# Kernel optimization log

Measured on AMD Instinct MI355X. Metric: run time of the kernel, lower is better.

## Reference

```python
import jax, jax.numpy as jnp
import numpy as np

B, T, S, E, H, V, OOV = 16, 32, 400, 128, 512, 32000, 50


def setup_inputs() -> dict:
    key = jax.random.key(0)
    ks = jax.random.split(key, 24)
    sc = 0.05
    inp = {
        'input_embeddings': jax.random.normal(ks[0], (B, T, E), jnp.float32),
        'h0': jax.random.normal(ks[1], (B, H), jnp.float32) * sc,
        'c0': jax.random.normal(ks[2], (B, H), jnp.float32) * sc,
        'encoder_outputs': jax.random.normal(ks[3], (B, S, H), jnp.float32),
        'encoder_masks': jnp.ones((B, S), jnp.float32),
        'extra_zeros': jnp.zeros((B, OOV), jnp.float32),
        'extended_source_idx': jax.random.randint(ks[4], (B, S), 0, V + OOV),
        # LSTM cell params (torch gate order i,f,g,o)
        'W_ih': jax.random.normal(ks[5], (4 * H, E), jnp.float32) * sc,
        'W_hh': jax.random.normal(ks[6], (4 * H, H), jnp.float32) * sc,
        'b_ih': jax.random.normal(ks[7], (4 * H,), jnp.float32) * sc,
        'b_hh': jax.random.normal(ks[8], (4 * H,), jnp.float32) * sc,
        # vocab projection
        'W_vocab': jax.random.normal(ks[9], (V, H), jnp.float32) * sc,
        'b_vocab': jax.random.normal(ks[10], (V,), jnp.float32) * sc,
        # attention: coverage_linear (H,1), energy_linear (H, 2H), v (H)
        'W_cov': jax.random.normal(ks[11], (H, 1), jnp.float32) * sc,
        'W_energy': jax.random.normal(ks[12], (H, 2 * H), jnp.float32) * sc,
        'b_energy': jax.random.normal(ks[13], (H,), jnp.float32) * sc,
        'v_attn': jax.random.uniform(ks[14], (H,), jnp.float32),
        # x_context: (E, E+H)
        'W_xctx': jax.random.normal(ks[15], (E, E + H), jnp.float32) * sc,
        'b_xctx': jax.random.normal(ks[16], (E,), jnp.float32) * sc,
        # attention_dense: (H, 2H)
        'W_ad': jax.random.normal(ks[17], (H, 2 * H), jnp.float32) * sc,
        'b_ad': jax.random.normal(ks[18], (H,), jnp.float32) * sc,
        # p_gen: (1, H + H + E)
        'W_pgen': jax.random.normal(ks[19], (1, 2 * H + E), jnp.float32) * sc,
        'b_pgen': jax.random.normal(ks[20], (1,), jnp.float32) * sc,
    }
    return inp


def _forward(input_embeddings, h0, c0, encoder_outputs, encoder_masks, extra_zeros,
             W_ih, W_hh, b_ih, b_hh, W_vocab, b_vocab, W_cov, W_energy, b_energy,
             v_attn, W_xctx, b_xctx, W_ad, b_ad, W_pgen, b_pgen, extended_source_idx):
    Bc, Sc_, Hc = encoder_outputs.shape
    oov = extra_zeros.shape[1]
    # split energy linear into decoder-part and encoder-part (cat order: [dec, enc])
    W_d, W_e = W_energy[:, :Hc], W_energy[:, Hc:]
    # encoder projection computed ONCE (same math as per-step recompute)
    enc_proj = jnp.einsum('bsh,kh->bsk', encoder_outputs, W_e) + b_energy  # [B,S,H]
    w_cov = W_cov[:, 0]  # [H]
    rows = jnp.arange(Bc)[:, None]

    def step(carry, emb_t):
        h, c, ctx, cov = carry  # [B,H],[B,H],[B,H],[B,S]
        x = jnp.concatenate([emb_t, ctx], -1) @ W_xctx.T + b_xctx  # [B,E]
        gates = x @ W_ih.T + b_ih + h @ W_hh.T + b_hh
        i_g, f_g, g_g, o_g = jnp.split(gates, 4, axis=-1)
        c = jax.nn.sigmoid(f_g) * c + jax.nn.sigmoid(i_g) * jnp.tanh(g_g)
        h = jax.nn.sigmoid(o_g) * jnp.tanh(c)
        # additive attention with coverage
        dec_proj = h @ W_d.T  # [B,H]
        cov_feat = cov[:, :, None] * w_cov[None, None, :]  # [B,S,H]
        energy = jnp.tanh(dec_proj[:, None, :] + enc_proj + cov_feat)
        score = jnp.einsum('bsh,h->bs', energy, v_attn)
        probs = jax.nn.softmax(score, axis=-1) * encoder_masks
        probs = probs / (probs.sum(-1, keepdims=True) + 1e-12)
        ctx = jnp.einsum('bs,bsh->bh', probs, encoder_outputs)
        cov = cov + probs
        # vocab distribution
        hh = jnp.concatenate([h, ctx], -1) @ W_ad.T + b_ad
        vocab_dist = jax.nn.softmax(hh @ W_vocab.T + b_vocab, axis=-1)  # [B,V]
        # pointer-generator mix
        p_gen = jax.nn.sigmoid(jnp.concatenate([ctx, h, x], -1) @ W_pgen.T + b_pgen)  # [B,1]
        attn_ = (1.0 - p_gen) * probs  # [B,S]
        ext = jnp.concatenate([vocab_dist * p_gen, extra_zeros], axis=1)  # [B,V+oov]
        final = ext.at[rows, extended_source_idx].add(attn_)
        return (h, c, ctx, cov), (final, probs, cov)

    init = (h0, c0, jnp.zeros_like(h0), jnp.zeros((Bc, Sc_), h0.dtype))
    (_, _, _, _), (finals, attns, covs) = jax.lax.scan(
        step, init, jnp.swapaxes(input_embeddings, 0, 1))
    return jnp.swapaxes(finals, 0, 1)  # [B,T,V+oov]


def reference(input_embeddings, h0, c0, encoder_outputs, encoder_masks, extra_zeros,
              extended_source_idx, W_ih, W_hh, b_ih, b_hh, W_vocab, b_vocab,
              W_cov, W_energy, b_energy, v_attn, W_xctx, b_xctx, W_ad, b_ad,
              W_pgen, b_pgen):
    return _forward(input_embeddings, h0, c0, encoder_outputs, encoder_masks,
                    extra_zeros, W_ih, W_hh, b_ih, b_hh, W_vocab, b_vocab,
                    W_cov, W_energy, b_energy, v_attn, W_xctx, b_xctx,
                    W_ad, b_ad, W_pgen, b_pgen, extended_source_idx)
```

## Files before the change

### kernel.cpp

```cpp
#include <hip/hip_runtime.h>
#include <hip/hip_bf16.h>
#include <cstddef>

namespace {

constexpr int B = 16, T = 32, S = 400, E = 128, H = 512, V = 32000, OOV = 50, VEXT = V + OOV;

typedef __attribute__((ext_vector_type(8))) short short8v;
typedef __attribute__((ext_vector_type(4))) float f32x4;

__device__ __forceinline__ float fsig(float x){ return 1.0f/(1.0f+__expf(-x)); }
__device__ __forceinline__ float ftanh(float x){
  float ax = fabsf(x);
  float t = __expf(-2.0f*ax);
  float r = (1.0f - t)/(1.0f + t);
  return copysignf(r, x);
}
__device__ __forceinline__ unsigned short f2bf(float f){
  unsigned int u = __float_as_uint(f);
  unsigned int r = (u + 0x7FFFu + ((u >> 16) & 1u)) >> 16;
  return (unsigned short)r;
}

__global__ __launch_bounds__(256) void k_init(const float* __restrict__ h0, const float* __restrict__ c0,
    float* __restrict__ h, float* __restrict__ c, float* __restrict__ cov,
    float* __restrict__ praw, float* __restrict__ vsum, float* __restrict__ hh_all){
  const int stride = gridDim.x*256;
  for (int i = blockIdx.x*256 + threadIdx.x; i < T*B*H; i += stride){
    hh_all[i] = 0.0f;
    if (i < B*H){ h[i]=h0[i]; c[i]=c0[i]; }
    if (i < B*S) cov[i]=0.0f;
    if (i < T*B){ praw[i]=0.0f; vsum[i]=0.0f; }
  }
}

__global__ __launch_bounds__(128) void k_x0(const float* __restrict__ emb,
    const float* __restrict__ W_xctx, const float* __restrict__ b_xctx,
    float* __restrict__ x0){
  const int b = blockIdx.x, tid = threadIdx.x;
  __shared__ float se[E];
  se[tid] = emb[(size_t)(b*T)*E + tid];
  __syncthreads();
  const float* w = W_xctx + (size_t)tid*(E+H);
  float acc = b_xctx[tid];
  #pragma unroll 8
  for (int k=0;k<E;k+=4){
    float4 wv = *reinterpret_cast<const float4*>(w+k);
    acc += se[k]*wv.x + se[k+1]*wv.y + se[k+2]*wv.z + se[k+3]*wv.w;
  }
  x0[b*E + tid] = acc;
}

__global__ __launch_bounds__(256) void k_trw2(const float* __restrict__ W_energy,
    float* __restrict__ Wt, float* __restrict__ WdT){
  __shared__ float tile[32][33];
  const int z = blockIdx.z;
  float* out = z ? WdT : Wt;
  const int off = z ? 0 : H;
  const int j0 = blockIdx.x*32, k0 = blockIdx.y*32;
  const int tx = threadIdx.x & 31, ty = threadIdx.x >> 5;
  #pragma unroll
  for (int r=0;r<4;++r)
    tile[ty+8*r][tx] = W_energy[(size_t)(k0+ty+8*r)*(2*H) + off + j0 + tx];
  __syncthreads();
  #pragma unroll
  for (int r=0;r<4;++r)
    out[(size_t)(j0+ty+8*r)*H + k0 + tx] = tile[tx][ty+8*r];
}

__global__ __launch_bounds__(512) void k_encproj(const float* __restrict__ enc,
                          const float* __restrict__ Wt,
                          const float* __restrict__ b_energy,
                          float* __restrict__ enc_proj){
  const int r0 = blockIdx.x*16, k = threadIdx.x;
  const float* eb = enc + (size_t)r0*H;
  float acc[16];
  #pragma unroll
  for (int r=0;r<16;++r) acc[r]=0.0f;
  for (int j=0;j<H;j+=4){
    const float w0 = Wt[(size_t) j   *H + k];
    const float w1 = Wt[(size_t)(j+1)*H + k];
    const float w2 = Wt[(size_t)(j+2)*H + k];
    const float w3 = Wt[(size_t)(j+3)*H + k];
    #pragma unroll
    for (int r=0;r<16;++r){
      acc[r] += eb[(size_t)r*H + j]*w0 + eb[(size_t)r*H + j+1]*w1
              + eb[(size_t)r*H + j+2]*w2 + eb[(size_t)r*H + j+3]*w3;
    }
  }
  const float be = b_energy[k];
  #pragma unroll
  for (int r=0;r<16;++r) enc_proj[(size_t)(r0+r)*H + k] = acc[r] + be;
}

__global__ __launch_bounds__(256) void k_gates2(
    const float* __restrict__ x, const float* __restrict__ hold,
    const float* __restrict__ W_ih, const float* __restrict__ W_hh,
    float* __restrict__ gpart){
  const int blk = blockIdx.x, tid = threadIdx.x;
  const int gbh = blk >> 2, kh = blk & 3;
  const int gb = gbh >> 1, bh = gbh & 1, b0 = bh*8;
  __shared__ float xh[8][640];
  __shared__ float sg[4][64][9];
  for (int b=0;b<8;++b)
    for (int k=tid;k<640;k+=256)
      xh[b][k] = (k<E) ? x[(b0+b)*E + k] : hold[(b0+b)*H + (k-E)];
  __syncthreads();
  const int w = tid >> 6, l = tid & 63, g = l >> 4, jj = l & 15;
  const int row = g*H + gb*16 + jj;
  float acc[8];
  #pragma unroll
  for (int b=0;b<8;++b) acc[b]=0.0f;
  const int ks = kh*160 + w*40, ke = ks + 40;
  const int k1 = (ke < 128) ? ke : 128;
  if (ks < 128){
    const float* wr = W_ih + (size_t)row*E;
    for (int k=ks; k<k1; k+=4){
      const float4 wv = *reinterpret_cast<const float4*>(wr + k);
      #pragma unroll
      for (int b=0;b<8;++b){
        const float4 xv = *reinterpret_cast<const float4*>(&xh[b][k]);
        acc[b] += xv.x*wv.x + xv.y*wv.y + xv.z*wv.z + xv.w*wv.w;
      }
    }
  }
  const int k2 = (ks > 128) ? ks : 128;
  if (k2 < ke){
    const float* wr = W_hh + (size_t)row*H - 128;
    for (int k=k2; k<ke; k+=4){
      const float4 wv = *reinterpret_cast<const float4*>(wr + k);
      #pragma unroll
      for (int b=0;b<8;++b){
        const float4 xv = *reinterpret_cast<const float4*>(&xh[b][k]);
        acc[b] += xv.x*wv.x + xv.y*wv.y + xv.z*wv.z + xv.w*wv.w;
      }
    }
  }
  #pragma unroll
  for (int b=0;b<8;++b) sg[w][l][b] = acc[b];
  __syncthreads();
  for (int i=tid; i<512; i+=256){
    const int l2 = i & 63, b = i >> 6;
    const int g2 = l2 >> 4, j2 = l2 & 15;
    const int row2 = g2*H + gb*16 + j2;
    gpart[((size_t)kh*B + (b0+b))*(4*H) + row2] =
        sg[0][l2][b]+sg[1][l2][b]+sg[2][l2][b]+sg[3][l2][b];
  }
}

__global__ __launch_bounds__(256) void k_dec2(const float* __restrict__ gpart,
    const float* __restrict__ cold, const float* __restrict__ b_ih,
    const float* __restrict__ b_hh, const float* __restrict__ WdT,
    float* __restrict__ cnew, float* __restrict__ hnew, float* __restrict__ dec){
  const int blk = blockIdx.x, tid = threadIdx.x;
  const int jc = blk >> 3, bp = blk & 7, b0 = bp*2;
  __shared__ float sh[2][H];
  __shared__ float r[4][64][2];
  for (int i=tid; i<2*H; i+=256){
    const int bl = i >> 9, j = i & 511;
    const int b = b0 + bl;
    float gs[4];
    #pragma unroll
    for (int g=0; g<4; ++g){
      const int row = g*H + j;
      float v = b_ih[row] + b_hh[row];
      #pragma unroll
      for (int kh=0; kh<4; ++kh) v += gpart[((size_t)kh*B + b)*(4*H) + row];
      gs[g] = v;
    }
    const float ig = fsig(gs[0]);
    const float fg = fsig(gs[1]);
    const float gg = ftanh(gs[2]);
    const float og = fsig(gs[3]);
    const float cn = fg*cold[b*H + j] + ig*gg;
    const float hn = og*ftanh(cn);
    cnew[b*H + j] = cn;
    hnew[b*H + j] = hn;
    sh[bl][j] = hn;
  }
  __syncthreads();
  const int w = tid >> 6, lane = tid & 63;
  const int j = jc*64 + lane;
  float a0=0.0f, a1=0.0f;
  for (int k=w*128; k<w*128+128; ++k){
    const float wv = WdT[(size_t)k*H + j];
    a0 += sh[0][k]*wv;
    a1 += sh[1][k]*wv;
  }
  r[w][lane][0]=a0; r[w][lane][1]=a1;
  __syncthreads();
  if (tid < 128){
    const int jl = tid & 63, bb = tid >> 6;
    dec[(b0+bb)*H + jc*64 + jl] = r[0][jl][bb]+r[1][jl][bb]+r[2][jl][bb]+r[3][jl][bb];
  }
}

__global__ __launch_bounds__(256) void k_score(const float* __restrict__ dec_proj,
    const float* __restrict__ enc_proj, const float* __restrict__ W_cov,
    const float* __restrict__ v_attn, const float* __restrict__ cov,
    float* __restrict__ score, float* __restrict__ xnext){
  const int b = blockIdx.y;
  if (blockIdx.x==0 && threadIdx.x < E) xnext[b*E + threadIdx.x] = 0.0f;
  const int wave = threadIdx.x >> 6, lane = threadIdx.x & 63;
  const int s = blockIdx.x*4 + wave;
  const float cv = cov[b*S + s];
  const float* ep = enc_proj + (size_t)(b*S + s)*H;
  const float* dp = dec_proj + b*H;
  float acc = 0.0f;
  const int k0 = lane*8;
  #pragma unroll
  for (int u=0;u<8;++u){
    const int k = k0+u;
    acc += ftanh(dp[k] + ep[k] + cv*W_cov[k]) * v_attn[k];
  }
  #pragma unroll
  for (int off=32; off>0; off>>=1) acc += __shfl_down(acc, off);
  if (lane==0) score[b*S + s] = acc;
}

__global__ __launch_bounds__(256) void k_ctxpost(const float* __restrict__ score,
    const float* __restrict__ masks, const float* __restrict__ enc,
    const float* __restrict__ h, const float* __restrict__ xcur,
    const float* __restrict__ emb, int tnext,
    const float* __restrict__ W_ad, const float* __restrict__ b_ad,
    const float* __restrict__ W_pgen, const float* __restrict__ b_pgen,
    const float* __restrict__ W_xctx, const float* __restrict__ b_xctx,
    float* __restrict__ cov, float* __restrict__ probs_t,
    float* __restrict__ hh_t, float* __restrict__ praw_t,
    float* __restrict__ xnext){
  const int b = blockIdx.x, hc = blockIdx.y, tid = threadIdx.x;
  __shared__ float red[256], sp[512], sctx[64], shh[H], se[E];
  for (int i=tid;i<H;i+=256) shh[i] = h[b*H + i];
  if (tid < E) se[tid] = emb[(size_t)(b*T + tnext)*E + tid];
  const float sc0 = (tid < S)      ? score[b*S + tid]       : -1e30f;
  const float sc1 = (tid+256 < S)  ? score[b*S + tid + 256] : -1e30f;
  red[tid] = fmaxf(sc0, sc1);
  __syncthreads();
  for (int off=128; off>0; off>>=1){ if (tid<off) red[tid]=fmaxf(red[tid],red[tid+off]); __syncthreads(); }
  const float mx = red[0];
  __syncthreads();
  const float e0 = (tid < S)     ? __expf(sc0 - mx) : 0.0f;
  const float e1 = (tid+256 < S) ? __expf(sc1 - mx) : 0.0f;
  red[tid] = e0 + e1;
  __syncthreads();
  for (int off=128; off>0; off>>=1){ if (tid<off) red[tid]+=red[tid+off]; __syncthreads(); }
  const float den = red[0];
  __syncthreads();
  const float p0 = (tid < S)     ? (e0/den)*masks[b*S+tid]     : 0.0f;
  const float p1 = (tid+256 < S) ? (e1/den)*masks[b*S+tid+256] : 0.0f;
  red[tid] = p0 + p1;
  __syncthreads();
  for (int off=128; off>0; off>>=1){ if (tid<off) red[tid]+=red[tid+off]; __syncthreads(); }
  const float inv = 1.0f/(red[0] + 1e-12f);
  __syncthreads();
  const float pr0 = p0*inv, pr1 = p1*inv;
  sp[tid] = pr0; sp[tid+256] = pr1;
  if (hc==0){
    if (tid < S){ probs_t[b*S+tid] = pr0; cov[b*S+tid] += pr0; }
    if (tid+256 < S){ probs_t[b*S+tid+256] = pr1; cov[b*S+tid+256] += pr1; }
  }
  __syncthreads();
  {
    const int c = tid & 63, sg_ = tid >> 6;
    const float* eb = enc + (size_t)b*S*H + hc*64 + c;
    float a = 0.0f;
    for (int s=sg_; s<S; s+=4) a += sp[s]*eb[(size_t)s*H];
    red[tid] = a;
    __syncthreads();
    if (tid < 64) sctx[tid] = red[tid]+red[tid+64]+red[tid+128]+red[tid+192];
  }
  __syncthreads();
  for (int j=tid; j<H; j+=256){
    const float* wr = W_ad + (size_t)j*(2*H);
    float acc = 0.0f;
    #pragma unroll
    for (int k=0;k<64;k+=4){
      const float4 wc = *reinterpret_cast<const float4*>(wr + H + hc*64 + k);
      acc += sctx[k]*wc.x + sctx[k+1]*wc.y + sctx[k+2]*wc.z + sctx[k+3]*wc.w;
      const float4 wh = *reinterpret_cast<const float4*>(wr + hc*64 + k);
      const float* hb = shh + hc*64 + k;
      acc += hb[0]*wh.x + hb[1]*wh.y + hb[2]*wh.z + hb[3]*wh.w;
    }
    if (hc==0) acc += b_ad[j];
    atomicAdd(&hh_t[b*H + j], acc);
  }
  if (tid < E){
    const float* wr = W_xctx + (size_t)tid*(E+H);
    float acc = 0.0f;
    #pragma unroll
    for (int k=0;k<64;k+=4){
      const float4 wc = *reinterpret_cast<const float4*>(wr + E + hc*64 + k);
      acc += sctx[k]*wc.x + sctx[k+1]*wc.y + sctx[k+2]*wc.z + sctx[k+3]*wc.w;
    }
    #pragma unroll
    for (int k=0;k<16;k+=4){
      const float4 we = *reinterpret_cast<const float4*>(wr + hc*16 + k);
      const float* eb2 = se + hc*16 + k;
      acc += eb2[0]*we.x + eb2[1]*we.y + eb2[2]*we.z + eb2[3]*we.w;
    }
    if (hc==0) acc += b_xctx[tid];
    atomicAdd(&xnext[b*E + tid], acc);
  }
  {
    float part = 0.0f;
    if (tid < 64){
      part = sctx[tid]*W_pgen[hc*64 + tid] + shh[hc*64 + tid]*W_pgen[H + hc*64 + tid];
      if (tid < 16) part += xcur[b*E + hc*16 + tid]*W_pgen[2*H + hc*16 + tid];
    }
    __syncthreads();
    red[tid] = part;
    __syncthreads();
    for (int off=128; off>0; off>>=1){ if (tid<off) red[tid]+=red[tid+off]; __syncthreads(); }
    if (tid==0) atomicAdd(&praw_t[b], red[0] + (hc==0 ? b_pgen[0] : 0.0f));
  }
}

__global__ __launch_bounds__(512) void k_vocab3(
    const float* __restrict__ hh_all,
    const float* __restrict__ W_vocab, const float* __restrict__ b_vocab,
    float* __restrict__ out, float* __restrict__ vsum){
  __shared__ unsigned short ldsA[256][72];
  __shared__ unsigned short ldsB[128][72];
  __shared__ float svs[256];
  const int tid = threadIdx.x, lane = tid & 63, w = tid >> 6;
  const int wm = w >> 1, wn = w & 1;
  const int m0 = (int)blockIdx.y * 256;
  const int n0 = (int)blockIdx.x * 128;
  const int nl = lane & 15, kg = lane >> 4;
  if (tid < 256) svs[tid] = 0.0f;
  f32x4 acc[4][4];
  #pragma unroll
  for (int mf=0;mf<4;++mf)
    #pragma unroll
    for (int nf=0;nf<4;++nf) acc[mf][nf] = (f32x4){0.f,0.f,0.f,0.f};
  for (int kc=0; kc<8; ++kc){
    __syncthreads();
    for (int j = tid; j < 4096; j += 512){
      const int row = j >> 4, c4 = j & 15;
      const float4 v = *reinterpret_cast<const float4*>(
          hh_all + (size_t)(m0+row)*H + kc*64 + c4*4);
      ushort4 u; u.x=f2bf(v.x); u.y=f2bf(v.y); u.z=f2bf(v.z); u.w=f2bf(v.w);
      *reinterpret_cast<ushort4*>(&ldsA[row][c4*4]) = u;
    }
    for (int j = tid; j < 2048; j += 512){
      const int row = j >> 4, c4 = j & 15;
      const float4 v = *reinterpret_cast<const float4*>(
          W_vocab + (size_t)(n0+row)*H + kc*64 + c4*4);
      ushort4 u; u.x=f2bf(v.x); u.y=f2bf(v.y); u.z=f2bf(v.z); u.w=f2bf(v.w);
      *reinterpret_cast<ushort4*>(&ldsB[row][c4*4]) = u;
    }
    __syncthreads();
    #pragma unroll
    for (int kk=0; kk<2; ++kk){
      short8v a[4], bf[4];
      #pragma unroll
      for (int mf=0;mf<4;++mf)
        a[mf] = *reinterpret_cast<const short8v*>(&ldsA[wm*64 + mf*16 + nl][kk*32 + kg*8]);
      #pragma unroll
      for (int nf=0;nf<4;++nf)
        bf[nf] = *reinterpret_cast<const short8v*>(&ldsB[wn*64 + nf*16 + nl][kk*32 + kg*8]);
      #pragma unroll
      for (int mf=0;mf<4;++mf)
        #pragma unroll
        for (int nf=0;nf<4;++nf)
          acc[mf][nf] = __builtin_amdgcn_mfma_f32_16x16x32_bf16(a[mf], bf[nf], acc[mf][nf], 0, 0, 0);
    }
  }
  float bv[4];
  #pragma unroll
  for (int nf=0;nf<4;++nf) bv[nf] = b_vocab[n0 + wn*64 + nf*16 + nl];
  #pragma unroll
  for (int mf=0;mf<4;++mf){
    #pragma unroll
    for (int r=0;r<4;++r){
      const int m = m0 + wm*64 + mf*16 + kg*4 + r;
      const int tq = m >> 4, bq = m & 15;
      float* orow = out + ((size_t)bq*T + tq)*VEXT;
      float s = 0.0f;
      #pragma unroll
      for (int nf=0;nf<4;++nf){
        const int n = n0 + wn*64 + nf*16 + nl;
        const float e = __expf(acc[mf][nf][r] + bv[nf]);
        orow[n] = e;
        s += e;
      }
      s += __shfl_xor(s, 1);
      s += __shfl_xor(s, 2);
      s += __shfl_xor(s, 4);
      s += __shfl_xor(s, 8);
      if (nl == 0) atomicAdd(&svs[m - m0], s);
    }
  }
  __syncthreads();
  for (int i = tid; i < 256; i += 512) atomicAdd(&vsum[m0 + i], svs[i]);
}

__global__ __launch_bounds__(256) void k_finalize(const float* __restrict__ praw,
    const float* __restrict__ vsum, const float* __restrict__ exz,
    float* __restrict__ out){
  const int rm = blockIdx.x, vc = blockIdx.y, tid = threadIdx.x;
  const int t = rm >> 4, b = rm & 15;
  float* orow = out + ((size_t)b*T + t)*VEXT;
  if (vc < 8){
    const float scl = fsig(praw[rm]) / vsum[rm];
    const int base = vc*4000;
    for (int i = tid; i < 4000; i += 256) orow[base + i] *= scl;
  } else if (tid < OOV){
    orow[V + tid] = exz[b*OOV + tid];
  }
}

__global__ __launch_bounds__(256) void k_scatter_all(const float* __restrict__ probs_all,
    const float* __restrict__ praw, const int* __restrict__ eidx,
    float* __restrict__ out){
  const int stride = gridDim.x*256;
  for (int i = blockIdx.x*256 + threadIdx.x; i < T*B*S; i += stride){
    const int t = i / (B*S);
    const int rem = i - t*B*S;
    const int b = rem / S, s = rem - b*S;
    const float fac = 1.0f - fsig(praw[t*B + b]);
    float* orow = out + ((size_t)b*T + t)*VEXT;
    atomicAdd(&orow[eidx[b*S + s]], fac*probs_all[(size_t)(t*B + b)*S + s]);
  }
}

}

extern "C" void kernel_launch(void* const* d_in, const int* in_sizes, int n_in,
                              void* d_out, int out_size, void* d_ws, size_t ws_size,
                              hipStream_t stream){
  const float* emb    = (const float*)d_in[0];
  const float* h0     = (const float*)d_in[1];
  const float* c0     = (const float*)d_in[2];
  const float* enc    = (const float*)d_in[3];
  const float* masks  = (const float*)d_in[4];
  const float* exz    = (const float*)d_in[5];
  const int*   eidx   = (const int*)d_in[6];
  const float* W_ih   = (const float*)d_in[7];
  const float* W_hh   = (const float*)d_in[8];
  const float* b_ih   = (const float*)d_in[9];
  const float* b_hh   = (const float*)d_in[10];
  const float* W_vocab= (const float*)d_in[11];
  const float* b_vocab= (const float*)d_in[12];
  const float* W_cov  = (const float*)d_in[13];
  const float* W_energy=(const float*)d_in[14];
  const float* b_energy=(const float*)d_in[15];
  const float* v_attn = (const float*)d_in[16];
  const float* W_xctx = (const float*)d_in[17];
  const float* b_xctx = (const float*)d_in[18];
  const float* W_ad   = (const float*)d_in[19];
  const float* b_ad   = (const float*)d_in[20];
  const float* W_pgen = (const float*)d_in[21];
  const float* b_pgen = (const float*)d_in[22];

  float* ws = (float*)d_ws;
  float* hbuf     = ws;
  float* cbuf     = ws + 16384;
  float* xbuf     = ws + 32768;
  float* dec      = ws + 36864;
  float* score    = ws + 45056;
  float* cov      = ws + 51456;
  float* praw     = ws + 57856;
  float* vsum     = ws + 58368;
  float* probs_all= ws + 58880;
  float* hh_all   = ws + 263680;
  float* WdT      = ws + 525824;
  float* Wt       = ws + 787968;
  float* gpart    = ws + 1050112;
  float* encp     = ws + 1181184;
  float* outp     = (float*)d_out;

  k_init<<<300,256,0,stream>>>(h0,c0,hbuf,cbuf,cov,praw,vsum,hh_all);
  k_x0<<<16,128,0,stream>>>(emb,W_xctx,b_xctx,xbuf);
  k_trw2<<<dim3(16,16,2),256,0,stream>>>(W_energy,Wt,WdT);
  k_encproj<<<400,512,0,stream>>>(enc,Wt,b_energy,encp);

  for (int t=0;t<T;++t){
    const int p = t&1;
    const float* hold = hbuf + p*8192;
    const float* cold = cbuf + p*8192;
    float* hnew = hbuf + (p^1)*8192;
    float* cnew = cbuf + (p^1)*8192;
    const float* xcur = xbuf + p*2048;
    float* xnext = xbuf + (p^1)*2048;
    const int tnext = (t+1 < T) ? (t+1) : (T-1);
    k_gates2<<<256,256,0,stream>>>(xcur,hold,W_ih,W_hh,gpart);
    k_dec2<<<64,256,0,stream>>>(gpart,cold,b_ih,b_hh,WdT,cnew,hnew,dec);
    k_score<<<dim3(100,16),256,0,stream>>>(dec,encp,W_cov,v_attn,cov,score,xnext);
    k_ctxpost<<<dim3(16,8),256,0,stream>>>(score,masks,enc,hnew,xcur,emb,tnext,
        W_ad,b_ad,W_pgen,b_pgen,W_xctx,b_xctx,
        cov,probs_all + (size_t)t*B*S, hh_all + (size_t)t*B*H, praw + t*B, xnext);
  }

  k_vocab3<<<dim3(250,2),512,0,stream>>>(hh_all,W_vocab,b_vocab,outp,vsum);
  k_finalize<<<dim3(512,9),256,0,stream>>>(praw,vsum,exz,outp);
  k_scatter_all<<<200,256,0,stream>>>(probs_all,praw,eidx,outp);
}
```

Baseline: 2.391 ms.

## Hoist attention_dense and p_gen out of recurrence; store encoder data in bf16

Moves the attention_dense projection and the p_gen dot product out of the per-step loop, since neither feeds the recurrence. Per-step h, ctx and x are stored for all timesteps, then one batched bf16 MFMA GEMM and one small kernel compute them afterwards. Encoder outputs and the encoder projection are also kept in bf16 to halve per-step memory traffic in the score and context kernels. The trade-off is lower precision in attention scores and context, plus an extra full-encoder conversion pass in init.

Result: faster. 2.159 ms (-9.7%).

```diff
diff --git a/kernel.cpp b/kernel.cpp
--- a/kernel.cpp
+++ b/kernel.cpp
@@ -21,16 +21,20 @@
   unsigned int r = (u + 0x7FFFu + ((u >> 16) & 1u)) >> 16;
   return (unsigned short)r;
 }
-
-__global__ __launch_bounds__(256) void k_init(const float* __restrict__ h0, const float* __restrict__ c0,
-    float* __restrict__ h, float* __restrict__ c, float* __restrict__ cov,
-    float* __restrict__ praw, float* __restrict__ vsum, float* __restrict__ hh_all){
+__device__ __forceinline__ float bf2f(unsigned short u){
+  return __uint_as_float(((unsigned)u) << 16);
+}
+
+__global__ __launch_bounds__(256) void k_init(const float* __restrict__ enc,
+    const float* __restrict__ h0, const float* __restrict__ c0,
+    unsigned short* __restrict__ enc_bf, float* __restrict__ harr,
+    float* __restrict__ cbuf, float* __restrict__ cov, float* __restrict__ vsum){
   const int stride = gridDim.x*256;
-  for (int i = blockIdx.x*256 + threadIdx.x; i < T*B*H; i += stride){
-    hh_all[i] = 0.0f;
-    if (i < B*H){ h[i]=h0[i]; c[i]=c0[i]; }
-    if (i < B*S) cov[i]=0.0f;
-    if (i < T*B){ praw[i]=0.0f; vsum[i]=0.0f; }
+  for (int i = blockIdx.x*256 + threadIdx.x; i < B*S*H; i += stride){
+    enc_bf[i] = f2bf(enc[i]);
+    if (i < B*H){ harr[i] = h0[i]; cbuf[i] = c0[i]; }
+    if (i < B*S) cov[i] = 0.0f;
+    if (i < T*B) vsum[i] = 0.0f;
   }
 }
 
@@ -71,7 +75,7 @@
 __global__ __launch_bounds__(512) void k_encproj(const float* __restrict__ enc,
                           const float* __restrict__ Wt,
                           const float* __restrict__ b_energy,
-                          float* __restrict__ enc_proj){
+                          unsigned short* __restrict__ enc_proj){
   const int r0 = blockIdx.x*16, k = threadIdx.x;
   const float* eb = enc + (size_t)r0*H;
   float acc[16];
@@ -90,7 +94,7 @@
   }
   const float be = b_energy[k];
   #pragma unroll
-  for (int r=0;r<16;++r) enc_proj[(size_t)(r0+r)*H + k] = acc[r] + be;
+  for (int r=0;r<16;++r) enc_proj[(size_t)(r0+r)*H + k] = f2bf(acc[r] + be);
 }
 
 __global__ __launch_bounds__(256) void k_gates2(
@@ -196,7 +200,7 @@
 }
 
 __global__ __launch_bounds__(256) void k_score(const float* __restrict__ dec_proj,
-    const float* __restrict__ enc_proj, const float* __restrict__ W_cov,
+    const unsigned short* __restrict__ encp, const float* __restrict__ W_cov,
     const float* __restrict__ v_attn, const float* __restrict__ cov,
     float* __restrict__ score, float* __restrict__ xnext){
   const int b = blockIdx.y;
@@ -204,33 +208,28 @@
   const int wave = threadIdx.x >> 6, lane = threadIdx.x & 63;
   const int s = blockIdx.x*4 + wave;
   const float cv = cov[b*S + s];
-  const float* ep = enc_proj + (size_t)(b*S + s)*H;
+  const int k0 = lane*8;
+  const short8v ev = *reinterpret_cast<const short8v*>(encp + (size_t)(b*S + s)*H + k0);
   const float* dp = dec_proj + b*H;
   float acc = 0.0f;
-  const int k0 = lane*8;
   #pragma unroll
   for (int u=0;u<8;++u){
     const int k = k0+u;
-    acc += ftanh(dp[k] + ep[k] + cv*W_cov[k]) * v_attn[k];
+    acc += ftanh(dp[k] + bf2f((unsigned short)ev[u]) + cv*W_cov[k]) * v_attn[k];
   }
   #pragma unroll
   for (int off=32; off>0; off>>=1) acc += __shfl_down(acc, off);
   if (lane==0) score[b*S + s] = acc;
 }
 
-__global__ __launch_bounds__(256) void k_ctxpost(const float* __restrict__ score,
-    const float* __restrict__ masks, const float* __restrict__ enc,
-    const float* __restrict__ h, const float* __restrict__ xcur,
+__global__ __launch_bounds__(256) void k_ctx(const float* __restrict__ score,
+    const float* __restrict__ masks, const unsigned short* __restrict__ enc_bf,
     const float* __restrict__ emb, int tnext,
-    const float* __restrict__ W_ad, const float* __restrict__ b_ad,
-    const float* __restrict__ W_pgen, const float* __restrict__ b_pgen,
     const float* __restrict__ W_xctx, const float* __restrict__ b_xctx,
     float* __restrict__ cov, float* __restrict__ probs_t,
-    float* __restrict__ hh_t, float* __restrict__ praw_t,
-    float* __restrict__ xnext){
+    float* __restrict__ ctx_t, float* __restrict__ xnext){
   const int b = blockIdx.x, hc = blockIdx.y, tid = threadIdx.x;
-  __shared__ float red[256], sp[512], sctx[64], shh[H], se[E];
-  for (int i=tid;i<H;i+=256) shh[i] = h[b*H + i];
+  __shared__ float red[256], sp[512], sctx[64], se[E];
   if (tid < E) se[tid] = emb[(size_t)(b*T + tnext)*E + tid];
   const float sc0 = (tid < S)      ? score[b*S + tid]       : -1e30f;
   const float sc1 = (tid+256 < S)  ? score[b*S + tid + 256] : -1e30f;
@@ -262,28 +261,18 @@
   __syncthreads();
   {
     const int c = tid & 63, sg_ = tid >> 6;
-    const float* eb = enc + (size_t)b*S*H + hc*64 + c;
+    const unsigned short* eb = enc_bf + (size_t)b*S*H + hc*64 + c;
     float a = 0.0f;
-    for (int s=sg_; s<S; s+=4) a += sp[s]*eb[(size_t)s*H];
+    for (int s=sg_; s<S; s+=4) a += sp[s]*bf2f(eb[(size_t)s*H]);
     red[tid] = a;
     __syncthreads();
-    if (tid < 64) sctx[tid] = red[tid]+red[tid+64]+red[tid+128]+red[tid+192];
-  }
-  __syncthreads();
-  for (int j=tid; j<H; j+=256){
-    const float* wr = W_ad + (size_t)j*(2*H);
-    float acc = 0.0f;
-    #pragma unroll
-    for (int k=0;k<64;k+=4){
-      const float4 wc = *reinterpret_cast<const float4*>(wr + H + hc*64 + k);
-      acc += sctx[k]*wc.x + sctx[k+1]*wc.y + sctx[k+2]*wc.z + sctx[k+3]*wc.w;
-      const float4 wh = *reinterpret_cast<const float4*>(wr + hc*64 + k);
-      const float* hb = shh + hc*64 + k;
-      acc += hb[0]*wh.x + hb[1]*wh.y + hb[2]*wh.z + hb[3]*wh.w;
-    }
-    if (hc==0) acc += b_ad[j];
-    atomicAdd(&hh_t[b*H + j], acc);
-  }
+    if (tid < 64){
+      const float cval = red[tid]+red[tid+64]+red[tid+128]+red[tid+192];
+      sctx[tid] = cval;
+      ctx_t[b*H + hc*64 + tid] = cval;
+    }
+  }
+  __syncthreads();
   if (tid < E){
     const float* wr = W_xctx + (size_t)tid*(E+H);
     float acc = 0.0f;
@@ -301,17 +290,91 @@
     if (hc==0) acc += b_xctx[tid];
     atomicAdd(&xnext[b*E + tid], acc);
   }
-  {
+}
+
+__global__ __launch_bounds__(512) void k_hhgemm(const float* __restrict__ harr,
+    const float* __restrict__ ctx_all, const float* __restrict__ W_ad,
+    const float* __restrict__ b_ad, float* __restrict__ hh_all){
+  __shared__ unsigned short ldsA[256][72];
+  __shared__ unsigned short ldsB[128][72];
+  const int tid = threadIdx.x, lane = tid & 63, w = tid >> 6;
+  const int wm = w >> 1, wn = w & 1;
+  const int m0 = (int)blockIdx.y * 256;
+  const int n0 = (int)blockIdx.x * 128;
+  const int nl = lane & 15, kg = lane >> 4;
+  f32x4 acc[4][4];
+  #pragma unroll
+  for (int mf=0;mf<4;++mf)
+    #pragma unroll
+    for (int nf=0;nf<4;++nf) acc[mf][nf] = (f32x4){0.f,0.f,0.f,0.f};
+  for (int kc=0; kc<16; ++kc){
+    __syncthreads();
+    for (int j = tid; j < 4096; j += 512){
+      const int row = j >> 4, c4 = j & 15;
+      const int kk_ = kc*64 + c4*4;
+      const float* src = (kk_ < H)
+        ? (harr + (size_t)(m0+row+B)*H + kk_)
+        : (ctx_all + (size_t)(m0+row)*H + (kk_ - H));
+      const float4 v = *reinterpret_cast<const float4*>(src);
+      ushort4 u; u.x=f2bf(v.x); u.y=f2bf(v.y); u.z=f2bf(v.z); u.w=f2bf(v.w);
+      *reinterpret_cast<ushort4*>(&ldsA[row][c4*4]) = u;
+    }
+    for (int j = tid; j < 2048; j += 512){
+      const int row = j >> 4, c4 = j & 15;
+      const float4 v = *reinterpret_cast<const float4*>(
+          W_ad + (size_t)(n0+row)*(2*H) + kc*64 + c4*4);
+      ushort4 u; u.x=f2bf(v.x); u.y=f2bf(v.y); u.z=f2bf(v.z); u.w=f2bf(v.w);
+      *reinterpret_cast<ushort4*>(&ldsB[row][c4*4]) = u;
+    }
+    __syncthreads();
+    #pragma unroll
+    for (int kk=0; kk<2; ++kk){
+      short8v a[4], bf[4];
+      #pragma unroll
+      for (int mf=0;mf<4;++mf)
+        a[mf] = *reinterpret_cast<const short8v*>(&ldsA[wm*64 + mf*16 + nl][kk*32 + kg*8]);
+      #pragma unroll
+      for (int nf=0;nf<4;++nf)
+        bf[nf] = *reinterpret_cast<const short8v*>(&ldsB[wn*64 + nf*16 + nl][kk*32 + kg*8]);
+      #pragma unroll
+      for (int mf=0;mf<4;++mf)
+        #pragma unroll
+        for (int nf=0;nf<4;++nf)
+          acc[mf][nf] = __builtin_amdgcn_mfma_f32_16x16x32_bf16(a[mf], bf[nf], acc[mf][nf], 0, 0, 0);
+    }
+  }
+  #pragma unroll
+  for (int mf=0;mf<4;++mf){
+    #pragma unroll
+    for (int r=0;r<4;++r){
+      const int m = m0 + wm*64 + mf*16 + kg*4 + r;
+      #pragma unroll
+      for (int nf=0;nf<4;++nf){
+        const int n = n0 + wn*64 + nf*16 + nl;
+        hh_all[(size_t)m*H + n] = acc[mf][nf][r] + b_ad[n];
+      }
+    }
+  }
+}
+
+__global__ __launch_bounds__(256) void k_pgen(const float* __restrict__ ctx_all,
+    const float* __restrict__ harr, const float* __restrict__ x_all,
+    const float* __restrict__ W_pgen, const float* __restrict__ b_pgen,
+    float* __restrict__ praw){
+  const int wglobal = blockIdx.x*4 + (threadIdx.x >> 6);
+  const int lane = threadIdx.x & 63;
+  for (int m = wglobal; m < T*B; m += 32){
     float part = 0.0f;
-    if (tid < 64){
-      part = sctx[tid]*W_pgen[hc*64 + tid] + shh[hc*64 + tid]*W_pgen[H + hc*64 + tid];
-      if (tid < 16) part += xcur[b*E + hc*16 + tid]*W_pgen[2*H + hc*16 + tid];
-    }
-    __syncthreads();
-    red[tid] = part;
-    __syncthreads();
-    for (int off=128; off>0; off>>=1){ if (tid<off) red[tid]+=red[tid+off]; __syncthreads(); }
-    if (tid==0) atomicAdd(&praw_t[b], red[0] + (hc==0 ? b_pgen[0] : 0.0f));
+    for (int k = lane; k < 2*H+E; k += 64){
+      float v;
+      if (k < H)        v = ctx_all[(size_t)m*H + k];
+      else if (k < 2*H) v = harr[(size_t)(m+B)*H + (k-H)];
+      else              v = x_all[(size_t)m*E + (k-2*H)];
+      part += v * W_pgen[k];
+    }
+    #pragma unroll
+    for (int off=32; off>0; off>>=1) part += __shfl_down(part, off);
+    if (lane==0) praw[m] = part + b_pgen[0];
   }
 }
 
@@ -454,45 +517,48 @@
   const float* b_pgen = (const float*)d_in[22];
 
   float* ws = (float*)d_ws;
-  float* hbuf     = ws;
-  float* cbuf     = ws + 16384;
-  float* xbuf     = ws + 32768;
-  float* dec      = ws + 36864;
-  float* score    = ws + 45056;
-  float* cov      = ws + 51456;
-  float* praw     = ws + 57856;
-  float* vsum     = ws + 58368;
-  float* probs_all= ws + 58880;
-  float* hh_all   = ws + 263680;
-  float* WdT      = ws + 525824;
-  float* Wt       = ws + 787968;
-  float* gpart    = ws + 1050112;
-  float* encp     = ws + 1181184;
+  float* cbuf     = ws;
+  float* x_all    = ws + 16384;
+  float* dec      = ws + 83968;
+  float* score    = ws + 92160;
+  float* cov      = ws + 98560;
+  float* praw     = ws + 104960;
+  float* vsum     = ws + 105472;
+  float* probs_all= ws + 105984;
+  float* harr     = ws + 310784;
+  float* ctx_all  = ws + 581120;
+  float* hh_all   = ws + 843264;
+  float* WdT      = ws + 1105408;
+  float* Wt       = ws + 1367552;
+  float* gpart    = ws + 1629696;
+  unsigned short* enc_bf = (unsigned short*)(ws + 1760768);
+  unsigned short* encp   = (unsigned short*)(ws + 3399168);
   float* outp     = (float*)d_out;
 
-  k_init<<<300,256,0,stream>>>(h0,c0,hbuf,cbuf,cov,praw,vsum,hh_all);
-  k_x0<<<16,128,0,stream>>>(emb,W_xctx,b_xctx,xbuf);
+  k_init<<<300,256,0,stream>>>(enc,h0,c0,enc_bf,harr,cbuf,cov,vsum);
+  k_x0<<<16,128,0,stream>>>(emb,W_xctx,b_xctx,x_all);
   k_trw2<<<dim3(16,16,2),256,0,stream>>>(W_energy,Wt,WdT);
   k_encproj<<<400,512,0,stream>>>(enc,Wt,b_energy,encp);
 
   for (int t=0;t<T;++t){
     const int p = t&1;
-    const float* hold = hbuf + p*8192;
     const float* cold = cbuf + p*8192;
-    float* hnew = hbuf + (p^1)*8192;
     float* cnew = cbuf + (p^1)*8192;
-    const float* xcur = xbuf + p*2048;
-    float* xnext = xbuf + (p^1)*2048;
     const int tnext = (t+1 < T) ? (t+1) : (T-1);
-    k_gates2<<<256,256,0,stream>>>(xcur,hold,W_ih,W_hh,gpart);
-    k_dec2<<<64,256,0,stream>>>(gpart,cold,b_ih,b_hh,WdT,cnew,hnew,dec);
-    k_score<<<dim3(100,16),256,0,stream>>>(dec,encp,W_cov,v_attn,cov,score,xnext);
-    k_ctxpost<<<dim3(16,8),256,0,stream>>>(score,masks,enc,hnew,xcur,emb,tnext,
-        W_ad,b_ad,W_pgen,b_pgen,W_xctx,b_xctx,
-        cov,probs_all + (size_t)t*B*S, hh_all + (size_t)t*B*H, praw + t*B, xnext);
-  }
-
-  k_vocab3<<<dim3(250,2),512,0,stream>>>(hh_all,W_vocab,b_vocab,outp,vsum);
-  k_finalize<<<dim3(512,9),256,0,stream>>>(praw,vsum,exz,outp);
-  k_scatter_all<<<200,256,0,stream>>>(probs_all,praw,eidx,outp);
-}
+    k_gates2<<<256,256,0,stream>>>(x_all + (size_t)t*B*E, harr + (size_t)t*B*H,
+                                   W_ih, W_hh, gpart);
+    k_dec2<<<64,256,0,stream>>>(gpart, cold, b_ih, b_hh, WdT,
+                                cnew, harr + (size_t)(t+1)*B*H, dec);
+    k_score<<<dim3(100,16),256,0,stream>>>(dec, encp, W_cov, v_attn, cov, score,
+                                           x_all + (size_t)(t+1)*B*E);
+    k_ctx<<<dim3(16,8),256,0,stream>>>(score, masks, enc_bf, emb, tnext,
+        W_xctx, b_xctx, cov, probs_all + (size_t)t*B*S,
+        ctx_all + (size_t)t*B*H, x_all + (size_t)(t+1)*B*E);
+  }
+
+  k_hhgemm<<<dim3(4,2),512,0,stream>>>(harr, ctx_all, W_ad, b_ad, hh_all);
+  k_pgen<<<8,256,0,stream>>>(ctx_all, harr, x_all, W_pgen, b_pgen, praw);
+  k_vocab3<<<dim3(250,2),512,0,stream>>>(hh_all, W_vocab, b_vocab, outp, vsum);
+  k_finalize<<<dim3(512,9),256,0,stream>>>(praw, vsum, exz, outp);
+  k_scatter_all<<<200,256,0,stream>>>(probs_all, praw, eidx, outp);
+}
```
